# Performance work log

Measured on AMD Instinct MI355X. Metric: run time of the kernel, lower is better.

The kernel has to match this reference:

```python
import jax, jax.numpy as jnp
import numpy as np
import math

M, N, D = 16384, 8192, 128
SIGMA = 1.0

def setup_inputs() -> dict:
    key = jax.random.key(0)
    k1, k2, k3 = jax.random.split(key, 3)
    x = jax.random.normal(k1, (M, D), dtype=jnp.float32)
    means = jax.random.normal(k2, (N, D), dtype=jnp.float32)
    weights = jax.random.uniform(k3, (N,), dtype=jnp.float32)
    return {"x": x, "means": means, "weights": weights}

def reference(x, means, weights):
    # GMM.eval_batch: cdist -> square -> gaussian kernel -> weighted sum
    var = SIGMA ** 2
    x = x.reshape(-1, means.shape[-1])
    x2 = jnp.sum(x * x, axis=-1, keepdims=True)            # (M,1)
    m2 = jnp.sum(means * means, axis=-1)                   # (N,)
    sq = jnp.maximum(x2 + m2[None, :] - 2.0 * (x @ means.T), 0.0)  # (M,N)
    coef = 1.0 / (2.0 * math.pi * var)
    dens = coef * jnp.exp(-sq / (2.0 * var))               # (M,N)
    return dens @ weights                                  # (M,)
```

## Files before the change

### kernel.cpp

```cpp
#include <hip/hip_runtime.h>
#include <math.h>

#define MM 16384
#define NN 8192
#define DD 128

#define L2E  1.4426950408889634f
#define COEF 0.15915494309189535f

__device__ __forceinline__ unsigned short f2h(float f) {
    _Float16 h = (_Float16)f;
    unsigned short u;
    __builtin_memcpy(&u, &h, 2);
    return u;
}

__device__ __forceinline__ void async16(short* lds, const short* g) {
    __builtin_amdgcn_global_load_lds(
        (const __attribute__((address_space(1))) unsigned int*)g,
        (__attribute__((address_space(3))) unsigned int*)lds,
        16, 0, 0);
}

typedef __attribute__((ext_vector_type(8))) _Float16 f16x8;
typedef __attribute__((ext_vector_type(4))) float f32x4;

__global__ __launch_bounds__(256) void gmm_prep_f16(
    const float* __restrict__ x, const float* __restrict__ means,
    const float* __restrict__ w, short* __restrict__ Acat,
    short* __restrict__ Bcat, float* __restrict__ xc, float* __restrict__ mc)
{
    const int tid  = threadIdx.x;
    const int rbk  = blockIdx.x;
    const bool isx = rbk < (MM / 16);
    const int rb   = isx ? rbk : rbk - (MM / 16);
    const int lane = tid & 63;
    const int rp   = (tid >> 6) * 4 + (lane >> 4);
    const int cg   = lane & 15;
    const int p    = cg >> 2;
    const int gk   = cg & 3;
    const int row  = rb * 16 + rp;

    const float* src = (isx ? x : means) + (size_t)row * DD + cg * 8;
    float4 u0 = ((const float4*)src)[0];
    float4 u1 = ((const float4*)src)[1];
    float a[8] = {u0.x, u0.y, u0.z, u0.w, u1.x, u1.y, u1.z, u1.w};

    float ss = 0.f;
    unsigned hi[4];
    #pragma unroll
    for (int q = 0; q < 4; ++q) {
        ss = fmaf(a[2 * q], a[2 * q], fmaf(a[2 * q + 1], a[2 * q + 1], ss));
        float a0 = isx ? a[2 * q] * L2E     : a[2 * q];
        float a1 = isx ? a[2 * q + 1] * L2E : a[2 * q + 1];
        hi[q] = (unsigned)f2h(a0) | ((unsigned)f2h(a1) << 16);
    }
    uint4 HI = make_uint4(hi[0], hi[1], hi[2], hi[3]);

    const int slot = rp * 4 + ((gk + (rp >> 1)) & 3);
    short* base = (isx ? Acat : Bcat) + (size_t)rb * 2048 + p * 512 + slot * 8;
    *(uint4*)base = HI;

    ss += __shfl_xor(ss, 1, 16);
    ss += __shfl_xor(ss, 2, 16);
    ss += __shfl_xor(ss, 4, 16);
    ss += __shfl_xor(ss, 8, 16);
    if (cg == 0) {
        if (isx) xc[row] = -0.5f * ss * L2E;
        else     mc[row] = (logf(w[row]) - 0.5f * ss) * L2E;
    }
}

__global__ __launch_bounds__(512, 4) void gmm_mfma(
    const short* __restrict__ Acat, const short* __restrict__ Bcat,
    const float* __restrict__ xc, const float* __restrict__ mc,
    float* __restrict__ out)
{
    __shared__ __align__(16) short smem[24576];
    __shared__ float red[4][128];

#define AS(b) (smem + (b) * 4096)
#define BS(b) (smem + 8192 + (b) * 8192)

    const int tid  = threadIdx.x;
    const int w    = tid >> 6, lane = tid & 63;
    const int wm   = w >> 2,   wn   = w & 3;
    const int quad = lane >> 4, col = lane & 15;
    const int m0   = blockIdx.x * 128;
    const int nb   = blockIdx.y * 256;

    const short* ga  = Acat + (size_t)(blockIdx.x * 8 + w) * 2048 + lane * 8;
    const short* gb0 = Bcat + (size_t)(blockIdx.y * 16 + w * 2) * 2048 + lane * 8;
    const short* gb1 = gb0 + 2048;
    const int aofs  = w * 512;
    const int bofs0 = w * 1024;
    const int bofs1 = w * 1024 + 512;

    float mcv[4];
    #pragma unroll
    for (int j = 0; j < 4; ++j) mcv[j] = mc[nb + wn * 64 + j * 16 + col];
    float xa[4][4];
    #pragma unroll
    for (int i = 0; i < 4; ++i) {
        float4 xv = *(const float4*)(xc + m0 + wm * 64 + i * 16 + quad * 4);
        xa[i][0] = xv.x; xa[i][1] = xv.y; xa[i][2] = xv.z; xa[i][3] = xv.w;
    }

    async16(AS(0) + aofs,  ga);
    async16(BS(0) + bofs0, gb0);
    async16(BS(0) + bofs1, gb1);

    f32x4 acc[4][4];
    #pragma unroll
    for (int i = 0; i < 4; ++i)
        #pragma unroll
        for (int j = 0; j < 4; ++j)
            acc[i][j] = (f32x4){xa[i][0] + mcv[j], xa[i][1] + mcv[j],
                                xa[i][2] + mcv[j], xa[i][3] + mcv[j]};

    const int rdo = col * 32 + ((quad + (col >> 1)) & 3) * 8;

    #pragma unroll 1
    for (int bk = 0; bk < 4; ++bk) {
        __syncthreads();
        if (bk < 3) {
            async16(AS((bk + 1) & 1) + aofs,  ga  + (bk + 1) * 512);
            async16(BS((bk + 1) & 1) + bofs0, gb0 + (bk + 1) * 512);
            async16(BS((bk + 1) & 1) + bofs1, gb1 + (bk + 1) * 512);
        }
        const short* as = AS(bk & 1);
        const short* bs = BS(bk & 1);
        f16x8 af[4];
        #pragma unroll
        for (int i = 0; i < 4; ++i)
            af[i] = *(const f16x8*)(as + (wm * 4 + i) * 512 + rdo);
        #pragma unroll
        for (int j = 0; j < 4; ++j) {
            f16x8 bfr = *(const f16x8*)(&bs[(wn * 4 + j) * 512 + rdo]);
            #pragma unroll
            for (int i = 0; i < 4; ++i)
                acc[i][j] = __builtin_amdgcn_mfma_f32_16x16x32_f16(
                    af[i], bfr, acc[i][j], 0, 0, 0);
        }
    }

    float sv[4][4];
    #pragma unroll
    for (int i = 0; i < 4; ++i) {
        #pragma unroll
        for (int r = 0; r < 4; ++r) {
            float s = 0.f;
            #pragma unroll
            for (int j = 0; j < 4; ++j)
                s += __builtin_exp2f(acc[i][j][r]);
            sv[i][r] = s;
        }
    }
    __syncthreads();
    {
        float* S = (float*)smem;
        const int p = wn * 16 + col;
        #pragma unroll
        for (int i = 0; i < 4; ++i) {
            const int mb = wm * 64 + i * 16 + quad * 4;
            #pragma unroll
            for (int r = 0; r < 4; ++r)
                S[(mb + r) * 68 + p] = sv[i][r];
        }
    }
    __syncthreads();
    {
        const float* S = (const float*)smem;
        const int m  = tid & 127;
        const int pg = tid >> 7;
        const float4* v = (const float4*)(S + m * 68 + pg * 16);
        float4 a0 = v[0], a1 = v[1], a2 = v[2], a3 = v[3];
        red[pg][m] = (a0.x + a0.y + a0.z + a0.w) + (a1.x + a1.y + a1.z + a1.w)
                   + (a2.x + a2.y + a2.z + a2.w) + (a3.x + a3.y + a3.z + a3.w);
    }
    __syncthreads();
    if (tid < 128)
        atomicAdd(out + m0 + tid,
                  COEF * (red[0][tid] + red[1][tid] + red[2][tid] + red[3][tid]));
#undef AS
#undef BS
}

__global__ __launch_bounds__(256) void gmm_prep(
    const float* __restrict__ x, const float* __restrict__ means,
    const float* __restrict__ w, float* __restrict__ xc, float* __restrict__ mc)
{
    int tid = blockIdx.x * 256 + threadIdx.x;
    if (tid < MM) {
        const float4* row = (const float4*)(x + (size_t)tid * DD);
        float ss = 0.f;
        #pragma unroll
        for (int i = 0; i < DD / 4; ++i) {
            float4 v = row[i];
            ss = fmaf(v.x, v.x, fmaf(v.y, v.y, fmaf(v.z, v.z, fmaf(v.w, v.w, ss))));
        }
        xc[tid] = -0.5f * ss * L2E;
    } else if (tid < MM + NN) {
        int n = tid - MM;
        const float4* row = (const float4*)(means + (size_t)n * DD);
        float ss = 0.f;
        #pragma unroll
        for (int i = 0; i < DD / 4; ++i) {
            float4 v = row[i];
            ss = fmaf(v.x, v.x, fmaf(v.y, v.y, fmaf(v.z, v.z, fmaf(v.w, v.w, ss))));
        }
        mc[n] = (logf(w[n]) - 0.5f * ss) * L2E;
    }
}

__global__ __launch_bounds__(256, 2) void gmm_main(
    const float* __restrict__ x, const float* __restrict__ means,
    const float* __restrict__ xc, const float* __restrict__ mc,
    float* __restrict__ out)
{
    __shared__ __align__(16) float Asm[128 * 128];
    __shared__ __align__(16) float Bsm[2][16 * 128];

    const int t   = threadIdx.x;
    const int tc  = t & 15;
    const int tr  = t >> 4;
    const int r0  = blockIdx.x * 128;
    const int nq0 = blockIdx.y * 2048;

    {
        float4 tmp[16];
        #pragma unroll
        for (int ii = 0; ii < 16; ++ii) {
            int idx = t + ii * 256;
            int r   = idx >> 5;
            int k0  = (idx & 31) << 2;
            tmp[ii] = *(const float4*)(x + (size_t)(r0 + r) * DD + k0);
        }
        #pragma unroll
        for (int ii = 0; ii < 16; ++ii) {
            int idx = t + ii * 256;
            int r   = idx >> 5;
            int k0  = (idx & 31) << 2;
            int rb  = r >> 3, rl = r & 7;
            float v[4] = {tmp[ii].x, tmp[ii].y, tmp[ii].z, tmp[ii].w};
            #pragma unroll
            for (int j = 0; j < 4; ++j) {
                int k = k0 + j;
                Asm[k * 128 + (((rb ^ (k & 15)) << 3) | rl)] = v[j];
            }
        }
    }

    float xcv[8];
    {
        float4 a = *(const float4*)(xc + r0 + tr * 8);
        float4 b = *(const float4*)(xc + r0 + tr * 8 + 4);
        xcv[0] = a.x; xcv[1] = a.y; xcv[2] = a.z; xcv[3] = a.w;
        xcv[4] = b.x; xcv[5] = b.y; xcv[6] = b.z; xcv[7] = b.w;
    }

    float rowAcc[8];
    #pragma unroll
    for (int i = 0; i < 8; ++i) rowAcc[i] = 0.f;

    for (int ntile = 0; ntile < 16; ++ntile) {
        const int nbase = nq0 + ntile * 128;

        float acc[8][8];
        #pragma unroll
        for (int i = 0; i < 8; ++i)
            #pragma unroll
            for (int j = 0; j < 8; ++j) acc[i][j] = 0.f;

        float4 ld[2];
        #pragma unroll
        for (int ii = 0; ii < 2; ++ii) {
            int flat = t + ii * 256;
            int nl   = flat >> 2;
            int kl   = (flat & 3) << 2;
            ld[ii] = *(const float4*)(means + (size_t)(nbase + nl) * DD + kl);
        }

        for (int ks = 0; ks < 8; ++ks) {
            const int buf = ks & 1;
            #pragma unroll
            for (int ii = 0; ii < 2; ++ii) {
                int flat = t + ii * 256;
                int nl   = flat >> 2;
                int k0   = (flat & 3) << 2;
                int nbk  = nl >> 3, nll = nl & 7;
                float v[4] = {ld[ii].x, ld[ii].y, ld[ii].z, ld[ii].w};
                #pragma unroll
                for (int j = 0; j < 4; ++j) {
                    int kl = k0 + j;
                    Bsm[buf][kl * 128 + (((nbk ^ kl) << 3) | nll)] = v[j];
                }
            }
            if (ks < 7) {
                #pragma unroll
                for (int ii = 0; ii < 2; ++ii) {
                    int flat = t + ii * 256;
                    int nl   = flat >> 2;
                    int kl   = (flat & 3) << 2;
                    ld[ii] = *(const float4*)(means + (size_t)(nbase + nl) * DD
                                              + (ks + 1) * 16 + kl);
                }
            }
            __syncthreads();

            #pragma unroll
            for (int kk = 0; kk < 16; ++kk) {
                const int k = ks * 16 + kk;
                const float* apx = &Asm[k * 128 + ((tr ^ kk) << 3)];
                float4 a0 = *(const float4*)apx;
                float4 a1 = *(const float4*)(apx + 4);
                const float* bpx = &Bsm[buf][kk * 128 + ((tc ^ kk) << 3)];
                float4 b0 = *(const float4*)bpx;
                float4 b1 = *(const float4*)(bpx + 4);
                float av[8] = {a0.x, a0.y, a0.z, a0.w, a1.x, a1.y, a1.z, a1.w};
                float bv[8] = {b0.x, b0.y, b0.z, b0.w, b1.x, b1.y, b1.z, b1.w};
                #pragma unroll
                for (int i = 0; i < 8; ++i)
                    #pragma unroll
                    for (int j = 0; j < 8; ++j)
                        acc[i][j] = fmaf(av[i], bv[j], acc[i][j]);
            }
        }

        float mcv[8];
        {
            float4 a = *(const float4*)(mc + nbase + tc * 8);
            float4 b = *(const float4*)(mc + nbase + tc * 8 + 4);
            mcv[0] = a.x; mcv[1] = a.y; mcv[2] = a.z; mcv[3] = a.w;
            mcv[4] = b.x; mcv[5] = b.y; mcv[6] = b.z; mcv[7] = b.w;
        }
        #pragma unroll
        for (int i = 0; i < 8; ++i) {
            float s = 0.f;
            #pragma unroll
            for (int j = 0; j < 8; ++j) {
                float arg = fmaf(acc[i][j], L2E, xcv[i] + mcv[j]);
                s += __builtin_exp2f(arg);
            }
            rowAcc[i] += s;
        }
    }

    #pragma unroll
    for (int i = 0; i < 8; ++i) {
        float v = rowAcc[i];
        v += __shfl_xor(v, 1, 16);
        v += __shfl_xor(v, 2, 16);
        v += __shfl_xor(v, 4, 16);
        v += __shfl_xor(v, 8, 16);
        if (tc == 0) atomicAdd(out + r0 + tr * 8 + i, COEF * v);
    }
}

extern "C" void kernel_launch(void* const* d_in, const int* in_sizes, int n_in,
                              void* d_out, int out_size, void* d_ws, size_t ws_size,
                              hipStream_t stream) {
    const float* x     = (const float*)d_in[0];
    const float* means = (const float*)d_in[1];
    const float* w     = (const float*)d_in[2];
    float* out = (float*)d_out;

    const size_t needA = (size_t)MM * 128 * sizeof(short);
    const size_t needB = (size_t)NN * 128 * sizeof(short);
    const size_t need  = needA + needB + (size_t)(MM + NN) * 4;

    if (ws_size >= need) {
        short* Acat = (short*)d_ws;
        short* Bcat = Acat + (size_t)MM * 128;
        float* xc   = (float*)(Bcat + (size_t)NN * 128);
        float* mc   = xc + MM;
        hipMemsetAsync(out, 0, MM * sizeof(float), stream);
        gmm_prep_f16<<<(MM + NN) / 16, 256, 0, stream>>>(x, means, w, Acat, Bcat, xc, mc);
        gmm_mfma<<<dim3(MM / 128, NN / 256), 512, 0, stream>>>(Acat, Bcat, xc, mc, out);
    } else {
        float* xc = (float*)d_ws;
        float* mc = xc + MM;
        hipMemsetAsync(out, 0, MM * sizeof(float), stream);
        gmm_prep<<<(MM + NN + 255) / 256, 256, 0, stream>>>(x, means, w, xc, mc);
        gmm_main<<<dim3(MM / 128, 4), 256, 0, stream>>>(x, means, xc, mc, out);
    }
}
```

Baseline: 126.1 us.

## Triple-buffer LDS tiles and unroll K-loop with explicit vmcnt waits

Replaces the double-buffered K loop with a three-stage LDS ring. Two tiles are now prefetched before compute starts, and the four K steps are fully unrolled, each guarded by an explicit s_waitcnt vmcnt and s_barrier. This lets global-to-LDS loads run further ahead of the MFMA work and removes loop overhead. The cost is more LDS per block (smem grows from 48KB to 72KB plus the reduction buffer), which may lower occupancy below the launch-bounds target. The hand-placed wait counts also have to match the outstanding loads exactly.

After: 123.3 us. -2.3%, faster.

```diff
diff --git a/kernel.cpp b/kernel.cpp
--- a/kernel.cpp
+++ b/kernel.cpp
@@ -76,11 +76,11 @@
     const float* __restrict__ xc, const float* __restrict__ mc,
     float* __restrict__ out)
 {
-    __shared__ __align__(16) short smem[24576];
+    __shared__ __align__(16) short smem[36864];
     __shared__ float red[4][128];
 
 #define AS(b) (smem + (b) * 4096)
-#define BS(b) (smem + 8192 + (b) * 8192)
+#define BS(b) (smem + 12288 + (b) * 8192)
 
     const int tid  = threadIdx.x;
     const int w    = tid >> 6, lane = tid & 63;
@@ -106,43 +106,74 @@
         xa[i][0] = xv.x; xa[i][1] = xv.y; xa[i][2] = xv.z; xa[i][3] = xv.w;
     }
 
+    f32x4 acc[4][4];
+    #pragma unroll
+    for (int i = 0; i < 4; ++i)
+        #pragma unroll
+        for (int j = 0; j < 4; ++j)
+            acc[i][j] = (f32x4){xa[i][0] + mcv[j], xa[i][1] + mcv[j],
+                                xa[i][2] + mcv[j], xa[i][3] + mcv[j]};
+
+    asm volatile("s_waitcnt vmcnt(0)" ::: "memory");
+    __builtin_amdgcn_sched_barrier(0);
+
     async16(AS(0) + aofs,  ga);
     async16(BS(0) + bofs0, gb0);
     async16(BS(0) + bofs1, gb1);
-
-    f32x4 acc[4][4];
-    #pragma unroll
-    for (int i = 0; i < 4; ++i)
-        #pragma unroll
-        for (int j = 0; j < 4; ++j)
-            acc[i][j] = (f32x4){xa[i][0] + mcv[j], xa[i][1] + mcv[j],
-                                xa[i][2] + mcv[j], xa[i][3] + mcv[j]};
+    async16(AS(1) + aofs,  ga  + 512);
+    async16(BS(1) + bofs0, gb0 + 512);
+    async16(BS(1) + bofs1, gb1 + 512);
 
     const int rdo = col * 32 + ((quad + (col >> 1)) & 3) * 8;
 
-    #pragma unroll 1
-    for (int bk = 0; bk < 4; ++bk) {
-        __syncthreads();
-        if (bk < 3) {
-            async16(AS((bk + 1) & 1) + aofs,  ga  + (bk + 1) * 512);
-            async16(BS((bk + 1) & 1) + bofs0, gb0 + (bk + 1) * 512);
-            async16(BS((bk + 1) & 1) + bofs1, gb1 + (bk + 1) * 512);
-        }
-        const short* as = AS(bk & 1);
-        const short* bs = BS(bk & 1);
-        f16x8 af[4];
-        #pragma unroll
-        for (int i = 0; i < 4; ++i)
-            af[i] = *(const f16x8*)(as + (wm * 4 + i) * 512 + rdo);
-        #pragma unroll
-        for (int j = 0; j < 4; ++j) {
-            f16x8 bfr = *(const f16x8*)(&bs[(wn * 4 + j) * 512 + rdo]);
-            #pragma unroll
-            for (int i = 0; i < 4; ++i)
-                acc[i][j] = __builtin_amdgcn_mfma_f32_16x16x32_f16(
-                    af[i], bfr, acc[i][j], 0, 0, 0);
-        }
-    }
+#define COMPUTE(as_, bs_)                                                     \
+    {                                                                         \
+        const short* as = (as_);                                              \
+        const short* bs = (bs_);                                              \
+        f16x8 af[4];                                                          \
+        _Pragma("unroll")                                                     \
+        for (int i = 0; i < 4; ++i)                                           \
+            af[i] = *(const f16x8*)(as + (wm * 4 + i) * 512 + rdo);           \
+        _Pragma("unroll")                                                     \
+        for (int j = 0; j < 4; ++j) {                                         \
+            f16x8 bfr = *(const f16x8*)(&bs[(wn * 4 + j) * 512 + rdo]);       \
+            _Pragma("unroll")                                                 \
+            for (int i = 0; i < 4; ++i)                                       \
+                acc[i][j] = __builtin_amdgcn_mfma_f32_16x16x32_f16(           \
+                    af[i], bfr, acc[i][j], 0, 0, 0);                          \
+        }                                                                     \
+    }
+
+    asm volatile("s_waitcnt vmcnt(3)" ::: "memory");
+    __builtin_amdgcn_sched_barrier(0);
+    __builtin_amdgcn_s_barrier();
+    __builtin_amdgcn_sched_barrier(0);
+    async16(AS(2) + aofs,  ga  + 1024);
+    async16(BS(2) + bofs0, gb0 + 1024);
+    async16(BS(2) + bofs1, gb1 + 1024);
+    COMPUTE(AS(0), BS(0));
+
+    asm volatile("s_waitcnt vmcnt(3)" ::: "memory");
+    __builtin_amdgcn_sched_barrier(0);
+    __builtin_amdgcn_s_barrier();
+    __builtin_amdgcn_sched_barrier(0);
+    async16(AS(0) + aofs,  ga  + 1536);
+    async16(BS(0) + bofs0, gb0 + 1536);
+    async16(BS(0) + bofs1, gb1 + 1536);
+    COMPUTE(AS(1), BS(1));
+
+    asm volatile("s_waitcnt vmcnt(3)" ::: "memory");
+    __builtin_amdgcn_sched_barrier(0);
+    __builtin_amdgcn_s_barrier();
+    __builtin_amdgcn_sched_barrier(0);
+    COMPUTE(AS(2), BS(2));
+
+    asm volatile("s_waitcnt vmcnt(0)" ::: "memory");
+    __builtin_amdgcn_sched_barrier(0);
+    __builtin_amdgcn_s_barrier();
+    __builtin_amdgcn_sched_barrier(0);
+    COMPUTE(AS(0), BS(0));
+#undef COMPUTE
 
     float sv[4][4];
     #pragma unroll
```

## Drop LDS staging; load MFMA fragments directly from global, shrink tiles, atomics per wave

Applied to the files above, without the earlier changes.

The MFMA kernel no longer stages A/B tiles in shared memory with async loads and barriers. Each wave now reads its f16 fragments straight from global memory in the pre-swizzled layout. The block tile shrinks to 128x128 with 256 threads, doubling the grid in N. The LDS cross-wave reduction is replaced by shuffle reductions and per-wave atomicAdds, which removes barriers but sends more atomics and repeated global/L2 fragment reads.

Result: slower. 140.3 us (+11.2%).

```diff
diff --git a/kernel.cpp b/kernel.cpp
--- a/kernel.cpp
+++ b/kernel.cpp
@@ -13,13 +13,6 @@
     unsigned short u;
     __builtin_memcpy(&u, &h, 2);
     return u;
-}
-
-__device__ __forceinline__ void async16(short* lds, const short* g) {
-    __builtin_amdgcn_global_load_lds(
-        (const __attribute__((address_space(1))) unsigned int*)g,
-        (__attribute__((address_space(3))) unsigned int*)lds,
-        16, 0, 0);
 }
 
 typedef __attribute__((ext_vector_type(8))) _Float16 f16x8;
@@ -71,30 +64,22 @@
     }
 }
 
-__global__ __launch_bounds__(512, 4) void gmm_mfma(
+__global__ __launch_bounds__(256, 3) void gmm_mfma(
     const short* __restrict__ Acat, const short* __restrict__ Bcat,
     const float* __restrict__ xc, const float* __restrict__ mc,
     float* __restrict__ out)
 {
-    __shared__ __align__(16) short smem[24576];
-    __shared__ float red[4][128];
-
-#define AS(b) (smem + (b) * 4096)
-#define BS(b) (smem + 8192 + (b) * 8192)
-
     const int tid  = threadIdx.x;
     const int w    = tid >> 6, lane = tid & 63;
-    const int wm   = w >> 2,   wn   = w & 3;
+    const int wm   = w >> 1,   wn   = w & 1;
     const int quad = lane >> 4, col = lane & 15;
     const int m0   = blockIdx.x * 128;
-    const int nb   = blockIdx.y * 256;
-
-    const short* ga  = Acat + (size_t)(blockIdx.x * 8 + w) * 2048 + lane * 8;
-    const short* gb0 = Bcat + (size_t)(blockIdx.y * 16 + w * 2) * 2048 + lane * 8;
-    const short* gb1 = gb0 + 2048;
-    const int aofs  = w * 512;
-    const int bofs0 = w * 1024;
-    const int bofs1 = w * 1024 + 512;
+    const int nb   = blockIdx.y * 128;
+
+    const int rdo = col * 32 + ((quad + (col >> 1)) & 3) * 8;
+
+    const short* ga = Acat + (size_t)(blockIdx.x * 8 + wm * 4) * 2048 + rdo;
+    const short* gb = Bcat + (size_t)(blockIdx.y * 8 + wn * 4) * 2048 + rdo;
 
     float mcv[4];
     #pragma unroll
@@ -106,10 +91,6 @@
         xa[i][0] = xv.x; xa[i][1] = xv.y; xa[i][2] = xv.z; xa[i][3] = xv.w;
     }
 
-    async16(AS(0) + aofs,  ga);
-    async16(BS(0) + bofs0, gb0);
-    async16(BS(0) + bofs1, gb1);
-
     f32x4 acc[4][4];
     #pragma unroll
     for (int i = 0; i < 4; ++i)
@@ -118,33 +99,23 @@
             acc[i][j] = (f32x4){xa[i][0] + mcv[j], xa[i][1] + mcv[j],
                                 xa[i][2] + mcv[j], xa[i][3] + mcv[j]};
 
-    const int rdo = col * 32 + ((quad + (col >> 1)) & 3) * 8;
-
-    #pragma unroll 1
+    #pragma unroll
     for (int bk = 0; bk < 4; ++bk) {
-        __syncthreads();
-        if (bk < 3) {
-            async16(AS((bk + 1) & 1) + aofs,  ga  + (bk + 1) * 512);
-            async16(BS((bk + 1) & 1) + bofs0, gb0 + (bk + 1) * 512);
-            async16(BS((bk + 1) & 1) + bofs1, gb1 + (bk + 1) * 512);
-        }
-        const short* as = AS(bk & 1);
-        const short* bs = BS(bk & 1);
-        f16x8 af[4];
+        f16x8 af[4], bf[4];
         #pragma unroll
         for (int i = 0; i < 4; ++i)
-            af[i] = *(const f16x8*)(as + (wm * 4 + i) * 512 + rdo);
-        #pragma unroll
-        for (int j = 0; j < 4; ++j) {
-            f16x8 bfr = *(const f16x8*)(&bs[(wn * 4 + j) * 512 + rdo]);
+            af[i] = *(const f16x8*)(ga + (size_t)i * 2048 + bk * 512);
+        #pragma unroll
+        for (int j = 0; j < 4; ++j)
+            bf[j] = *(const f16x8*)(gb + (size_t)j * 2048 + bk * 512);
+        #pragma unroll
+        for (int j = 0; j < 4; ++j)
             #pragma unroll
             for (int i = 0; i < 4; ++i)
                 acc[i][j] = __builtin_amdgcn_mfma_f32_16x16x32_f16(
-                    af[i], bfr, acc[i][j], 0, 0, 0);
-        }
-    }
-
-    float sv[4][4];
+                    af[i], bf[j], acc[i][j], 0, 0, 0);
+    }
+
     #pragma unroll
     for (int i = 0; i < 4; ++i) {
         #pragma unroll
@@ -153,37 +124,14 @@
             #pragma unroll
             for (int j = 0; j < 4; ++j)
                 s += __builtin_exp2f(acc[i][j][r]);
-            sv[i][r] = s;
-        }
-    }
-    __syncthreads();
-    {
-        float* S = (float*)smem;
-        const int p = wn * 16 + col;
-        #pragma unroll
-        for (int i = 0; i < 4; ++i) {
-            const int mb = wm * 64 + i * 16 + quad * 4;
-            #pragma unroll
-            for (int r = 0; r < 4; ++r)
-                S[(mb + r) * 68 + p] = sv[i][r];
-        }
-    }
-    __syncthreads();
-    {
-        const float* S = (const float*)smem;
-        const int m  = tid & 127;
-        const int pg = tid >> 7;
-        const float4* v = (const float4*)(S + m * 68 + pg * 16);
-        float4 a0 = v[0], a1 = v[1], a2 = v[2], a3 = v[3];
-        red[pg][m] = (a0.x + a0.y + a0.z + a0.w) + (a1.x + a1.y + a1.z + a1.w)
-                   + (a2.x + a2.y + a2.z + a2.w) + (a3.x + a3.y + a3.z + a3.w);
-    }
-    __syncthreads();
-    if (tid < 128)
-        atomicAdd(out + m0 + tid,
-                  COEF * (red[0][tid] + red[1][tid] + red[2][tid] + red[3][tid]));
-#undef AS
-#undef BS
+            s += __shfl_xor(s, 1, 16);
+            s += __shfl_xor(s, 2, 16);
+            s += __shfl_xor(s, 4, 16);
+            s += __shfl_xor(s, 8, 16);
+            if (col == 0)
+                atomicAdd(out + m0 + wm * 64 + i * 16 + quad * 4 + r, COEF * s);
+        }
+    }
 }
 
 __global__ __launch_bounds__(256) void gmm_prep(
@@ -376,7 +324,7 @@
         float* mc   = xc + MM;
         hipMemsetAsync(out, 0, MM * sizeof(float), stream);
         gmm_prep_f16<<<(MM + NN) / 16, 256, 0, stream>>>(x, means, w, Acat, Bcat, xc, mc);
-        gmm_mfma<<<dim3(MM / 128, NN / 256), 512, 0, stream>>>(Acat, Bcat, xc, mc, out);
+        gmm_mfma<<<dim3(MM / 128, NN / 128), 256, 0, stream>>>(Acat, Bcat, xc, mc, out);
     } else {
         float* xc = (float*)d_ws;
         float* mc = xc + MM;
```
